# Optimization experiments

Measured on AMD Instinct MI355X. Metric: run time of the kernel, lower is better.

Reference implementation:

```python
import jax, jax.numpy as jnp
import numpy as np
from jax import lax

B, T, N_MELS = 8, 4096, 26
W_FRAMES = 32          # window_frames
CONV_CH, CONV_K = 64, 5
SE_MID = CONV_CH // 4  # se_ratio=4 on feature_dim=conv_channels
H1, H2 = 256, 128      # hidden_dims
SHORT_W, SHORT_H = 8, 128
OUT_CH = 2             # downbeat=True


def setup_inputs() -> dict:
    key = jax.random.key(0)
    ks = jax.random.split(key, 16)
    s = lambda *sh: 1.0 / np.sqrt(sh[0])
    return {
        "x": jax.random.normal(ks[0], (B, T, N_MELS), jnp.float32),
        # conv1d: kernel stored (K, in, out) for NWC/WIO conv
        "conv_w": jax.random.normal(ks[1], (CONV_K, N_MELS, CONV_CH), jnp.float32) * 0.1,
        "conv_b": jax.random.normal(ks[2], (CONV_CH,), jnp.float32) * 0.1,
        # SE on feature_dim=CONV_CH
        "se_w1": jax.random.normal(ks[3], (CONV_CH, SE_MID), jnp.float32) * s(CONV_CH),
        "se_b1": jnp.zeros((SE_MID,), jnp.float32),
        "se_w2": jax.random.normal(ks[4], (SE_MID, CONV_CH), jnp.float32) * s(SE_MID),
        "se_b2": jnp.zeros((CONV_CH,), jnp.float32),
        # long backbone: (W_FRAMES*CONV_CH) -> H1 -> H2
        "w1": jax.random.normal(ks[5], (W_FRAMES * CONV_CH, H1), jnp.float32) * s(W_FRAMES * CONV_CH),
        "b1": jnp.zeros((H1,), jnp.float32),
        "w2": jax.random.normal(ks[6], (H1, H2), jnp.float32) * s(H1),
        "b2": jnp.zeros((H2,), jnp.float32),
        # short backbone: (SHORT_W*CONV_CH) -> SHORT_H
        "sw": jax.random.normal(ks[7], (SHORT_W * CONV_CH, SHORT_H), jnp.float32) * s(SHORT_W * CONV_CH),
        "sb": jnp.zeros((SHORT_H,), jnp.float32),
        # output head: (H2 + SHORT_H) -> OUT_CH
        "wo": jax.random.normal(ks[8], (H2 + SHORT_H, OUT_CH), jnp.float32) * s(H2 + SHORT_H),
        "bo": jnp.zeros((OUT_CH,), jnp.float32),
    }


def reference(x, conv_w, conv_b, se_w1, se_b1, se_w2, se_b2,
              w1, b1, w2, b2, sw, sb, wo, bo):
    batch, time, _ = x.shape
    # 1) causal conv1d over full sequence (left-pad K-1), then ReLU
    xp = jnp.pad(x, ((0, 0), (CONV_K - 1, 0), (0, 0)))
    xc = lax.conv_general_dilated(xp, conv_w, window_strides=(1,),
                                  padding='VALID',
                                  dimension_numbers=('NWC', 'WIO', 'NWC'))
    xc = jax.nn.relu(xc + conv_b)                      # (B, T, F=CONV_CH)
    # 2) causal sliding-window unfold: windows[b,t,w,:] = padded[b, t+w, :]
    x_pad = jnp.pad(xc, ((0, 0), (W_FRAMES - 1, 0), (0, 0)))
    idx = jnp.arange(time)[:, None] + jnp.arange(W_FRAMES)[None, :]
    windows = x_pad[:, idx, :]                          # (B, T, W, F)
    # 3) SE channel attention (pool over window dim)
    s = windows.mean(axis=2)                            # (B, T, F)
    a = jax.nn.sigmoid(jax.nn.relu(s @ se_w1 + se_b1) @ se_w2 + se_b2)
    windows = windows * a[:, :, None, :]
    # 4) long backbone (dropout = identity in eval)
    flat_long = windows.reshape(batch, time, W_FRAMES * CONV_CH)
    h = jax.nn.relu(flat_long @ w1 + b1)
    h = jax.nn.relu(h @ w2 + b2)                        # (B, T, H2)
    # short path: last SHORT_W frames of the same SE-processed window
    flat_short = windows[:, :, -SHORT_W:, :].reshape(batch, time, SHORT_W * CONV_CH)
    h_short = jax.nn.relu(flat_short @ sw + sb)         # (B, T, SHORT_H)
    h = jnp.concatenate([h, h_short], axis=-1)
    # 5) output head
    return jax.nn.sigmoid(h @ wo + bo)                  # (B, T, OUT_CH)
```

## Files before the change

### kernel.cpp

```cpp
#include <hip/hip_runtime.h>

typedef _Float16 half_t;
typedef __attribute__((ext_vector_type(8))) _Float16 h8;
typedef __attribute__((ext_vector_type(2))) _Float16 h2v;
typedef __attribute__((ext_vector_type(4))) float f4;
typedef __attribute__((ext_vector_type(2))) float f2v;

__device__ __forceinline__ half_t to_h(float v) {
    v = fminf(fmaxf(v, -60000.f), 60000.f);
    return (half_t)v;
}

__global__ void pack_k(const float* __restrict__ w1, const float* __restrict__ w2,
                       const float* __restrict__ sw, const float* __restrict__ cw,
                       half_t* __restrict__ wsH) {
    int i = blockIdx.x * 256 + threadIdx.x;
    if (i < 65536) {
        int L = i & 63, nt = (i >> 6) & 15, kk = i >> 10;
        int k0 = kk * 32 + ((L >> 4) << 3), n = (nt << 4) + (L & 15);
        h8 v;
#pragma unroll
        for (int j = 0; j < 8; j++) v[j] = to_h(w1[(k0 + j) * 256 + n]);
        *(h8*)(wsH + ((((kk * 16 + nt) * 64 + L)) << 3)) = v;
    } else if (i < 69632) {
        int o = i - 65536;
        int L = o & 63, nt = (o >> 6) & 7, kk = o >> 9;
        int k0 = kk * 32 + ((L >> 4) << 3), n = (nt << 4) + (L & 15);
        h8 v;
#pragma unroll
        for (int j = 0; j < 8; j++) v[j] = to_h(w2[(k0 + j) * 128 + n]);
        *(h8*)(wsH + 524288 + ((((kk * 8 + nt) * 64 + L)) << 3)) = v;
    } else if (i < 77824) {
        int o = i - 69632;
        int L = o & 63, nt = (o >> 6) & 7, kk = o >> 9;
        int k0 = kk * 32 + ((L >> 4) << 3), n = (nt << 4) + (L & 15);
        h8 v;
#pragma unroll
        for (int j = 0; j < 8; j++) v[j] = to_h(sw[(k0 + j) * 128 + n]);
        *(h8*)(wsH + 557056 + ((((kk * 8 + nt) * 64 + L)) << 3)) = v;
    } else if (i < 79104) {
        int o = i - 77824;
        int L = o & 63, nt = (o >> 6) & 3, k5 = o >> 8;
        int n = nt * 16 + (L & 15);
        h8 v;
#pragma unroll
        for (int j = 0; j < 8; j++) {
            int kin = ((L >> 4) << 3) + j;
            v[j] = (kin < 26) ? to_h(cw[(k5 * 26 + kin) * 64 + n]) : (half_t)0.f;
        }
        *(h8*)(wsH + 622592 + ((size_t)o << 3)) = v;
    }
}

#define XCS 72
#define XLS 32
#define ALS 72
#define Y1S 264
#define SLS 68
#define HLS 20

#define MFMA16(a, b, c) __builtin_amdgcn_mfma_f32_16x16x32_f16(a, b, c, 0, 0, 0)

__global__ __launch_bounds__(512, 4) void beat_main(
    const float* __restrict__ x,
    const float* __restrict__ conv_b,
    const float* __restrict__ se_w1, const float* __restrict__ se_b1,
    const float* __restrict__ se_w2, const float* __restrict__ se_b2,
    const float* __restrict__ b1, const float* __restrict__ b2,
    const float* __restrict__ sb,
    const float* __restrict__ wo, const float* __restrict__ bo,
    const half_t* __restrict__ w1p, const half_t* __restrict__ w2p,
    const half_t* __restrict__ swp, const half_t* __restrict__ cwB,
    float* __restrict__ out) {

    __shared__ __align__(16) char smem[58752];
    half_t* xcL = (half_t*)smem;
    half_t* aL  = (half_t*)(smem + 13696);
    char*   U   = smem + 22912;
    half_t* xLh = (half_t*)U;
    float*  sLf = (float*)U;
    float*  hidL= (float*)(U + 17408);
    half_t* y1L = (half_t*)U;
    float*  woL = (float*)(smem + 56704);

    const int tid = threadIdx.x;
    const int bi = blockIdx.x;
    const int b = bi >> 6;
    const int t0 = (bi & 63) << 6;
    const int lane = tid & 63, wv = tid >> 6;
    const int quad = lane >> 4, rl = lane & 15;

    if (tid < 256) ((f2v*)woL)[tid] = ((const f2v*)wo)[tid];
    for (int idx = tid; idx < 99 * 13; idx += 512) {
        int fi = idx / 13, ip = idx - fi * 13;
        int tx = t0 - 35 + fi;
        h2v v;
        if (tx >= 0) {
            const float* xp = x + ((size_t)(b * 4096 + tx)) * 26 + 2 * ip;
            v[0] = to_h(xp[0]); v[1] = to_h(xp[1]);
        } else { v[0] = (_Float16)0.f; v[1] = (_Float16)0.f; }
        *(h2v*)(xLh + fi * XLS + 2 * ip) = v;
    }
    for (int idx = tid; idx < 99 * 3; idx += 512) {
        int fi = idx / 3, p = idx - fi * 3;
        h2v z; z[0] = (_Float16)0.f; z[1] = (_Float16)0.f;
        *(h2v*)(xLh + fi * XLS + 26 + 2 * p) = z;
    }
    __syncthreads();

    {
        const h8* cwv = (const h8*)cwB;
#pragma unroll
        for (int s = 0; s < 3; s++) {
            int u = wv + 8 * s;
            int rb = u >> 2, nt = u & 3;
            f4 acc;
#pragma unroll
            for (int r = 0; r < 4; r++) acc[r] = 0.f;
#pragma unroll
            for (int k5 = 0; k5 < 5; k5++) {
                h8 xv = *(const h8*)(xLh + (rb * 16 + rl + k5) * XLS + quad * 8);
                h8 bf = cwv[(k5 * 4 + nt) * 64 + lane];
                acc = MFMA16(xv, bf, acc);
            }
            int n = nt * 16 + rl;
            float bias = conv_b[n];
#pragma unroll
            for (int r = 0; r < 4; r++) {
                int m = rb * 16 + quad * 4 + r;
                if (m < 95) {
                    int t = t0 - 31 + m;
                    float v = (t >= 0) ? fmaxf(acc[r] + bias, 0.f) : 0.f;
                    xcL[m * XCS + n] = to_h(v);
                }
            }
        }
    }
    __syncthreads();

    {
        int m = tid >> 3, cg = tid & 7;
        const half_t* base = xcL + m * XCS + cg * 8;
        f4 a0, a1;
#pragma unroll
        for (int r = 0; r < 4; r++) { a0[r] = 0.f; a1[r] = 0.f; }
#pragma unroll
        for (int w = 0; w < 32; w++) {
            h8 v = *(const h8*)(base + w * XCS);
#pragma unroll
            for (int q = 0; q < 4; q++) { a0[q] += (float)v[q]; a1[q] += (float)v[4 + q]; }
        }
        float* sp = sLf + m * SLS + cg * 8;
        *(f4*)sp       = a0 * (1.f / 32.f);
        *(f4*)(sp + 4) = a1 * (1.f / 32.f);
    }
    __syncthreads();

    {
        int m = tid >> 3, hh = (tid & 7) * 2;
        float acc0 = se_b1[hh], acc1 = se_b1[hh + 1];
        for (int c = 0; c < 64; c++) {
            float sv = sLf[m * SLS + c];
            f2v wq = *(const f2v*)(se_w1 + c * 16 + hh);
            acc0 += sv * wq[0]; acc1 += sv * wq[1];
        }
        hidL[m * HLS + hh] = fmaxf(acc0, 0.f);
        hidL[m * HLS + hh + 1] = fmaxf(acc1, 0.f);
    }
    __syncthreads();

    {
        int m = tid >> 3, c0 = (tid & 7) * 8;
        float av[8];
#pragma unroll
        for (int j = 0; j < 8; j++) av[j] = se_b2[c0 + j];
        for (int h = 0; h < 16; h++) {
            float hv = hidL[m * HLS + h];
            const f4* wv4 = (const f4*)(se_w2 + h * 64 + c0);
            f4 wq0 = wv4[0], wq1 = wv4[1];
#pragma unroll
            for (int j = 0; j < 4; j++) { av[j] += hv * wq0[j]; av[4 + j] += hv * wq1[j]; }
        }
#pragma unroll
        for (int j = 0; j < 8; j++) {
            float zz = fminf(fmaxf(av[j], -30.f), 30.f);
            float s = 1.f / (1.f + __expf(-zz));
            aL[m * ALS + c0 + j] = to_h(s);
        }
    }
    __syncthreads();

    h8 avr[4][2];
#pragma unroll
    for (int mt = 0; mt < 4; mt++)
#pragma unroll
        for (int p = 0; p < 2; p++)
            avr[mt][p] = *(const h8*)(aL + (mt * 16 + rl) * ALS + p * 32 + quad * 8);

    {
        f4 acc[4][2];
#pragma unroll
        for (int mt = 0; mt < 4; mt++)
#pragma unroll
            for (int i = 0; i < 2; i++)
#pragma unroll
                for (int r = 0; r < 4; r++) acc[mt][i][r] = 0.f;
        const h8* w1v = (const h8*)w1p;
        const int fb = wv * 2;
        h8 bA[2], bB[2], bC[2], bD[2];
#pragma unroll
        for (int i = 0; i < 2; i++) bA[i] = w1v[(fb + i) * 64 + lane];
#pragma unroll
        for (int i = 0; i < 2; i++) bB[i] = w1v[(16 + fb + i) * 64 + lane];
#pragma unroll 2
        for (int kk = 0; kk < 64; kk += 2) {
            const int k2 = (kk + 2) & 63, k3 = (kk + 3) & 63;
#pragma unroll
            for (int i = 0; i < 2; i++) bC[i] = w1v[(k2 * 16 + fb + i) * 64 + lane];
#pragma unroll
            for (int i = 0; i < 2; i++) bD[i] = w1v[(k3 * 16 + fb + i) * 64 + lane];
            const int wf = kk >> 1;
            {
                const int c0 = quad * 8;
#pragma unroll
                for (int mt = 0; mt < 4; mt++) {
                    int m = mt * 16 + rl;
                    h8 xv = *(const h8*)(xcL + (m + wf) * XCS + c0);
                    h8 af = xv * avr[mt][0];
                    acc[mt][0] = MFMA16(af, bA[0], acc[mt][0]);
                    acc[mt][1] = MFMA16(af, bA[1], acc[mt][1]);
                }
            }
            {
                const int c0 = 32 + quad * 8;
#pragma unroll
                for (int mt = 0; mt < 4; mt++) {
                    int m = mt * 16 + rl;
                    h8 xv = *(const h8*)(xcL + (m + wf) * XCS + c0);
                    h8 af = xv * avr[mt][1];
                    acc[mt][0] = MFMA16(af, bB[0], acc[mt][0]);
                    acc[mt][1] = MFMA16(af, bB[1], acc[mt][1]);
                }
            }
#pragma unroll
            for (int i = 0; i < 2; i++) { bA[i] = bC[i]; bB[i] = bD[i]; }
        }
#pragma unroll
        for (int i = 0; i < 2; i++) {
            int n = wv * 32 + i * 16 + rl;
            float bb = b1[n];
#pragma unroll
            for (int mt = 0; mt < 4; mt++)
#pragma unroll
                for (int r = 0; r < 4; r++) {
                    int m = mt * 16 + quad * 4 + r;
                    y1L[m * Y1S + n] = to_h(fmaxf(acc[mt][i][r] + bb, 0.f));
                }
        }
    }
    __syncthreads();

    f4 acc2[4];
#pragma unroll
    for (int mt = 0; mt < 4; mt++)
#pragma unroll
        for (int r = 0; r < 4; r++) acc2[mt][r] = 0.f;
    {
        const h8* w2v = (const h8*)w2p;
        h8 cf = w2v[wv * 64 + lane];
#pragma unroll 2
        for (int kk = 0; kk < 8; kk++) {
            int kn = (kk + 1) & 7;
            h8 nf = w2v[(kn * 8 + wv) * 64 + lane];
#pragma unroll
            for (int mt = 0; mt < 4; mt++) {
                h8 av = *(const h8*)(y1L + (mt * 16 + rl) * Y1S + kk * 32 + quad * 8);
                acc2[mt] = MFMA16(av, cf, acc2[mt]);
            }
            cf = nf;
        }
    }

    f4 accS[4];
#pragma unroll
    for (int mt = 0; mt < 4; mt++)
#pragma unroll
        for (int r = 0; r < 4; r++) accS[mt][r] = 0.f;
    {
        const h8* swv = (const h8*)swp;
        h8 cf = swv[wv * 64 + lane];
#pragma unroll 2
        for (int kk = 0; kk < 16; kk++) {
            int kn = (kk + 1) & 15;
            h8 nf = swv[(kn * 8 + wv) * 64 + lane];
            const int wf = 24 + (kk >> 1);
            const int c0 = ((kk & 1) << 5) + quad * 8;
#pragma unroll
            for (int mt = 0; mt < 4; mt++) {
                int m = mt * 16 + rl;
                h8 xv = *(const h8*)(xcL + (m + wf) * XCS + c0);
                h8 af = xv * avr[mt][kk & 1];
                accS[mt] = MFMA16(af, cf, accS[mt]);
            }
            cf = nf;
        }
    }
    __syncthreads();

    {
        int n = wv * 16 + rl;
        float bb2 = b2[n], bbs = sb[n];
#pragma unroll
        for (int mt = 0; mt < 4; mt++)
#pragma unroll
            for (int r = 0; r < 4; r++) {
                int m = mt * 16 + quad * 4 + r;
                y1L[m * Y1S + n]       = to_h(fmaxf(acc2[mt][r] + bb2, 0.f));
                y1L[m * Y1S + 128 + n] = to_h(fmaxf(accS[mt][r] + bbs, 0.f));
            }
    }
    __syncthreads();

    if (tid < 128) {
        int m = tid >> 1, o = tid & 1;
        float z = bo[o];
        const half_t* hrow = y1L + m * Y1S;
        for (int nb = 0; nb < 32; nb++) {
            h8 hv = *(const h8*)(hrow + nb * 8);
#pragma unroll
            for (int q = 0; q < 8; q++)
                z += (float)hv[q] * woL[(nb * 8 + q) * 2 + o];
        }
        z = fminf(fmaxf(z, -30.f), 30.f);
        float sg = 1.f / (1.f + __expf(-z));
        out[((size_t)(b * 4096 + t0 + m)) * 2 + o] = sg;
    }
}

extern "C" void kernel_launch(void* const* d_in, const int* in_sizes, int n_in,
                              void* d_out, int out_size, void* d_ws, size_t ws_size,
                              hipStream_t stream) {
    const float* x      = (const float*)d_in[0];
    const float* conv_w = (const float*)d_in[1];
    const float* conv_b = (const float*)d_in[2];
    const float* se_w1  = (const float*)d_in[3];
    const float* se_b1  = (const float*)d_in[4];
    const float* se_w2  = (const float*)d_in[5];
    const float* se_b2  = (const float*)d_in[6];
    const float* w1     = (const float*)d_in[7];
    const float* b1     = (const float*)d_in[8];
    const float* w2     = (const float*)d_in[9];
    const float* b2     = (const float*)d_in[10];
    const float* sw     = (const float*)d_in[11];
    const float* sb     = (const float*)d_in[12];
    const float* wo     = (const float*)d_in[13];
    const float* bo     = (const float*)d_in[14];
    half_t* wsH = (half_t*)d_ws;

    hipLaunchKernelGGL(pack_k, dim3(337), dim3(256), 0, stream, w1, w2, sw, conv_w, wsH);
    hipLaunchKernelGGL(beat_main, dim3(512), dim3(512), 0, stream,
                       x, conv_b, se_w1, se_b1, se_w2, se_b2, b1, b2, sb, wo, bo,
                       wsH, wsH + 524288, wsH + 557056, wsH + 622592,
                       (float*)d_out);
}
```

Before: 140.9 us.

## Fuse short-path GEMM into long GEMM tail and reduce output head via shuffles

The short-backbone MFMAs now run inside the last quarter of the W1 K-loop, since both use the same SE-scaled A fragments of the last 8 frames. This removes a separate pass that reloaded xcL and recomputed the scaling. The output head is computed in registers: each wave dots its hidden slice with wo, reduces across 16 lanes with xor shuffles, and writes partial sums to a small shared buffer that 128 threads then sum over waves. This drops the fp16 write of the hidden layer, one __syncthreads, the woL staging and about 2 KB of LDS. The cost is extra registers held live during the W1 loop, which may raise VGPR pressure against launch_bounds(512,4).

Measured after the change: 146.5 us. 1.04x slower.

```diff
diff --git a/kernel.cpp b/kernel.cpp
--- a/kernel.cpp
+++ b/kernel.cpp
@@ -73,15 +73,15 @@
     const half_t* __restrict__ swp, const half_t* __restrict__ cwB,
     float* __restrict__ out) {
 
-    __shared__ __align__(16) char smem[58752];
+    __shared__ __align__(16) char smem[56704];
     half_t* xcL = (half_t*)smem;
     half_t* aL  = (half_t*)(smem + 13696);
+    float*  zbuf= (float*)(smem + 13696);
     char*   U   = smem + 22912;
     half_t* xLh = (half_t*)U;
     float*  sLf = (float*)U;
     float*  hidL= (float*)(U + 17408);
     half_t* y1L = (half_t*)U;
-    float*  woL = (float*)(smem + 56704);
 
     const int tid = threadIdx.x;
     const int bi = blockIdx.x;
@@ -90,7 +90,6 @@
     const int lane = tid & 63, wv = tid >> 6;
     const int quad = lane >> 4, rl = lane & 15;
 
-    if (tid < 256) ((f2v*)woL)[tid] = ((const f2v*)wo)[tid];
     for (int idx = tid; idx < 99 * 13; idx += 512) {
         int fi = idx / 13, ip = idx - fi * 13;
         int tx = t0 - 35 + fi;
@@ -197,6 +196,12 @@
         for (int p = 0; p < 2; p++)
             avr[mt][p] = *(const h8*)(aL + (mt * 16 + rl) * ALS + p * 32 + quad * 8);
 
+    f4 accS[4];
+#pragma unroll
+    for (int mt = 0; mt < 4; mt++)
+#pragma unroll
+        for (int r = 0; r < 4; r++) accS[mt][r] = 0.f;
+    f4 acc2[4];
     {
         f4 acc[4][2];
 #pragma unroll
@@ -206,6 +211,7 @@
 #pragma unroll
                 for (int r = 0; r < 4; r++) acc[mt][i][r] = 0.f;
         const h8* w1v = (const h8*)w1p;
+        const h8* swv = (const h8*)swp;
         const int fb = wv * 2;
         h8 bA[2], bB[2], bC[2], bD[2];
 #pragma unroll
@@ -213,8 +219,8 @@
 #pragma unroll
         for (int i = 0; i < 2; i++) bB[i] = w1v[(16 + fb + i) * 64 + lane];
 #pragma unroll 2
-        for (int kk = 0; kk < 64; kk += 2) {
-            const int k2 = (kk + 2) & 63, k3 = (kk + 3) & 63;
+        for (int kk = 0; kk < 48; kk += 2) {
+            const int k2 = kk + 2, k3 = kk + 3;
 #pragma unroll
             for (int i = 0; i < 2; i++) bC[i] = w1v[(k2 * 16 + fb + i) * 64 + lane];
 #pragma unroll
@@ -245,6 +251,44 @@
 #pragma unroll
             for (int i = 0; i < 2; i++) { bA[i] = bC[i]; bB[i] = bD[i]; }
         }
+#pragma unroll 2
+        for (int kk = 48; kk < 64; kk += 2) {
+            const int k2 = (kk + 2) & 63, k3 = (kk + 3) & 63;
+#pragma unroll
+            for (int i = 0; i < 2; i++) bC[i] = w1v[(k2 * 16 + fb + i) * 64 + lane];
+#pragma unroll
+            for (int i = 0; i < 2; i++) bD[i] = w1v[(k3 * 16 + fb + i) * 64 + lane];
+            const int ks = kk - 48;
+            h8 s0 = swv[(ks * 8 + wv) * 64 + lane];
+            h8 s1 = swv[((ks + 1) * 8 + wv) * 64 + lane];
+            const int wf = kk >> 1;
+            {
+                const int c0 = quad * 8;
+#pragma unroll
+                for (int mt = 0; mt < 4; mt++) {
+                    int m = mt * 16 + rl;
+                    h8 xv = *(const h8*)(xcL + (m + wf) * XCS + c0);
+                    h8 af = xv * avr[mt][0];
+                    acc[mt][0] = MFMA16(af, bA[0], acc[mt][0]);
+                    acc[mt][1] = MFMA16(af, bA[1], acc[mt][1]);
+                    accS[mt]   = MFMA16(af, s0, accS[mt]);
+                }
+            }
+            {
+                const int c0 = 32 + quad * 8;
+#pragma unroll
+                for (int mt = 0; mt < 4; mt++) {
+                    int m = mt * 16 + rl;
+                    h8 xv = *(const h8*)(xcL + (m + wf) * XCS + c0);
+                    h8 af = xv * avr[mt][1];
+                    acc[mt][0] = MFMA16(af, bB[0], acc[mt][0]);
+                    acc[mt][1] = MFMA16(af, bB[1], acc[mt][1]);
+                    accS[mt]   = MFMA16(af, s1, accS[mt]);
+                }
+            }
+#pragma unroll
+            for (int i = 0; i < 2; i++) { bA[i] = bC[i]; bB[i] = bD[i]; }
+        }
 #pragma unroll
         for (int i = 0; i < 2; i++) {
             int n = wv * 32 + i * 16 + rl;
@@ -260,7 +304,6 @@
     }
     __syncthreads();
 
-    f4 acc2[4];
 #pragma unroll
     for (int mt = 0; mt < 4; mt++)
 #pragma unroll
@@ -281,42 +324,30 @@
         }
     }
 
-    f4 accS[4];
-#pragma unroll
-    for (int mt = 0; mt < 4; mt++)
-#pragma unroll
-        for (int r = 0; r < 4; r++) accS[mt][r] = 0.f;
-    {
-        const h8* swv = (const h8*)swp;
-        h8 cf = swv[wv * 64 + lane];
-#pragma unroll 2
-        for (int kk = 0; kk < 16; kk++) {
-            int kn = (kk + 1) & 15;
-            h8 nf = swv[(kn * 8 + wv) * 64 + lane];
-            const int wf = 24 + (kk >> 1);
-            const int c0 = ((kk & 1) << 5) + quad * 8;
-#pragma unroll
-            for (int mt = 0; mt < 4; mt++) {
-                int m = mt * 16 + rl;
-                h8 xv = *(const h8*)(xcL + (m + wf) * XCS + c0);
-                h8 af = xv * avr[mt][kk & 1];
-                accS[mt] = MFMA16(af, cf, accS[mt]);
-            }
-            cf = nf;
-        }
-    }
-    __syncthreads();
-
     {
         int n = wv * 16 + rl;
         float bb2 = b2[n], bbs = sb[n];
+        f2v wt = *(const f2v*)(wo + n * 2);
+        f2v ws = *(const f2v*)(wo + (128 + n) * 2);
+        float* zb = zbuf + wv * 128;
 #pragma unroll
         for (int mt = 0; mt < 4; mt++)
 #pragma unroll
             for (int r = 0; r < 4; r++) {
-                int m = mt * 16 + quad * 4 + r;
-                y1L[m * Y1S + n]       = to_h(fmaxf(acc2[mt][r] + bb2, 0.f));
-                y1L[m * Y1S + 128 + n] = to_h(fmaxf(accS[mt][r] + bbs, 0.f));
+                float h2 = fmaxf(acc2[mt][r] + bb2, 0.f);
+                float hs = fmaxf(accS[mt][r] + bbs, 0.f);
+                float z0 = h2 * wt[0] + hs * ws[0];
+                float z1 = h2 * wt[1] + hs * ws[1];
+#pragma unroll
+                for (int s = 1; s < 16; s <<= 1) {
+                    z0 += __shfl_xor(z0, s, 64);
+                    z1 += __shfl_xor(z1, s, 64);
+                }
+                if (rl == 0) {
+                    int m = mt * 16 + quad * 4 + r;
+                    zb[m * 2]     = z0;
+                    zb[m * 2 + 1] = z1;
+                }
             }
     }
     __syncthreads();
@@ -324,13 +355,8 @@
     if (tid < 128) {
         int m = tid >> 1, o = tid & 1;
         float z = bo[o];
-        const half_t* hrow = y1L + m * Y1S;
-        for (int nb = 0; nb < 32; nb++) {
-            h8 hv = *(const h8*)(hrow + nb * 8);
-#pragma unroll
-            for (int q = 0; q < 8; q++)
-                z += (float)hv[q] * woL[(nb * 8 + q) * 2 + o];
-        }
+#pragma unroll
+        for (int w = 0; w < 8; w++) z += zbuf[w * 128 + m * 2 + o];
         z = fminf(fmaxf(z, -30.f), 30.f);
         float sg = 1.f / (1.f + __expf(-z));
         out[((size_t)(b * 4096 + t0 + m)) * 2 + o] = sg;
```
